# Kernel tuning notes

Hardware: AMD Instinct MI355X
Metric: run time of the kernel (lower is better)

The kernel has to match this reference:

```python
import jax, jax.numpy as jnp
import numpy as np

N = 200000; E = 800000; B = 4096; L = 512
DIN = 64; DE = 16; H = 128; PD = 1152


def setup_inputs() -> dict:
    key = jax.random.key(0)
    ks = jax.random.split(key, 40)
    def nrm(k, shape, fan_in):
        return jax.random.normal(k, shape, jnp.float32) * (1.0 / np.sqrt(fan_in))
    inp = {}
    inp['x'] = jax.random.normal(ks[0], (N, DIN), jnp.float32)
    inp['edge_index'] = jax.random.randint(ks[1], (2, E), 0, N, dtype=jnp.int32)
    inp['edge_attr'] = jax.random.normal(ks[2], (E, DE), jnp.float32)
    inp['batch'] = jnp.sort(jax.random.randint(ks[3], (N,), 0, B, dtype=jnp.int32))
    # 6 expert blocks: [0,1]=shared, [2,3]=sars, [4,5]=mers
    inp['eW1'] = nrm(ks[4], (6, DIN, H), DIN); inp['ea_s1'] = nrm(ks[5], (6, H), H)
    inp['ea_d1'] = nrm(ks[6], (6, H), H); inp['eWe1'] = nrm(ks[7], (6, DE, H), DE)
    inp['ea_e1'] = nrm(ks[8], (6, H), H); inp['eb1'] = jnp.zeros((6, H), jnp.float32)
    inp['bn1_g'] = jnp.ones((6, H), jnp.float32); inp['bn1_b'] = jnp.zeros((6, H), jnp.float32)
    inp['eW2'] = nrm(ks[9], (6, H, H), H); inp['ea_s2'] = nrm(ks[10], (6, H), H)
    inp['ea_d2'] = nrm(ks[11], (6, H), H); inp['eWe2'] = nrm(ks[12], (6, DE, H), DE)
    inp['ea_e2'] = nrm(ks[13], (6, H), H); inp['eb2'] = jnp.zeros((6, H), jnp.float32)
    inp['bn2_g'] = jnp.ones((6, H), jnp.float32); inp['bn2_b'] = jnp.zeros((6, H), jnp.float32)
    # gates (one GATConv with 4 output channels per task)
    inp['gW'] = nrm(ks[14], (2, DIN, 4), DIN); inp['ga_s'] = nrm(ks[15], (2, 4), 4)
    inp['ga_d'] = nrm(ks[16], (2, 4), 4); inp['gWe'] = nrm(ks[17], (2, DE, 4), DE)
    inp['ga_e'] = nrm(ks[18], (2, 4), 4); inp['gb'] = jnp.zeros((2, 4), jnp.float32)
    # cross-modal attention per task + frozen protein embeddings
    inp['Wq'] = nrm(ks[19], (2, H, H), H)
    inp['Wk'] = nrm(ks[20], (2, PD, H), PD)
    inp['Wv'] = nrm(ks[21], (2, PD, H), PD)
    inp['pe'] = jax.random.normal(ks[22], (2, L, PD), jnp.float32)
    # task heads
    inp['Wh1'] = nrm(ks[23], (2, 2 * H, H), 2 * H); inp['bh1'] = jnp.zeros((2, H), jnp.float32)
    inp['hbn_g'] = jnp.ones((2, H), jnp.float32); inp['hbn_b'] = jnp.zeros((2, H), jnp.float32)
    inp['Wh2'] = nrm(ks[24], (2, H, 1), H); inp['bh2'] = jnp.zeros((2, 1), jnp.float32)
    return inp


def _gat(x, src, dst, eattr, W, a_s, a_d, We, a_e, b):
    # PyG GATConv (heads=1, edge_dim set): shared linear for src/dst.
    h = x @ W                                   # [N, C]
    l = (h @ a_s)[src] + (h @ a_d)[dst] + (eattr @ We) @ a_e  # [E]
    l = jax.nn.leaky_relu(l, 0.2)
    m = jax.ops.segment_max(l, dst, num_segments=N)
    m = jnp.where(jnp.isfinite(m), m, 0.0)
    ex = jnp.exp(l - m[dst])
    den = jax.ops.segment_sum(ex, dst, num_segments=N)
    alpha = ex / (den[dst] + 1e-16)             # edge softmax over incoming edges
    return jax.ops.segment_sum(alpha[:, None] * h[src], dst, num_segments=N) + b


def _gat_multi(x, src, dst, eattr, W, a_s, a_d, We, a_e, b):
    # gate GATConv outputs C>1 channels with heads=1 -> same scalar-alpha math
    return _gat(x, src, dst, eattr, W, a_s, a_d, We, a_e, b)


def _bn(x, g, b):
    mu = jnp.mean(x, axis=0)
    var = jnp.var(x, axis=0)
    return (x - mu) * jax.lax.rsqrt(var + 1e-5) * g + b


def reference(x, edge_index, edge_attr, batch,
              eW1, ea_s1, ea_d1, eWe1, ea_e1, eb1, bn1_g, bn1_b,
              eW2, ea_s2, ea_d2, eWe2, ea_e2, eb2, bn2_g, bn2_b,
              gW, ga_s, ga_d, gWe, ga_e, gb,
              Wq, Wk, Wv, pe, Wh1, bh1, hbn_g, hbn_b, Wh2, bh2):
    src, dst = edge_index[0], edge_index[1]

    def expert(i):
        h = _gat(x, src, dst, edge_attr, eW1[i], ea_s1[i], ea_d1[i], eWe1[i], ea_e1[i], eb1[i])
        h = jax.nn.leaky_relu(_bn(h, bn1_g[i], bn1_b[i]), 0.01)
        h = _gat(h, src, dst, edge_attr, eW2[i], ea_s2[i], ea_d2[i], eWe2[i], ea_e2[i], eb2[i])
        return jax.nn.leaky_relu(_bn(h, bn2_g[i], bn2_b[i]), 0.01)

    reps = [expert(i) for i in range(6)]  # each [N, H]

    preds = []
    for t in range(2):
        # merged experts: shared then task-specific (cat order in torch code)
        merged = jnp.stack([reps[0], reps[1], reps[2 + 2 * t], reps[3 + 2 * t]], axis=1)  # [N,4,H]
        glog = _gat_multi(x, src, dst, edge_attr, gW[t], ga_s[t], ga_d[t], gWe[t], ga_e[t], gb[t])
        gate = jax.nn.softmax(glog, axis=1)                     # [N,4]
        node = jnp.einsum('neh,ne->nh', merged, gate)           # CGC combine
        pooled = jax.ops.segment_sum(node, batch, num_segments=B)  # global_add_pool [B,H]
        Q = pooled @ Wq[t]                                      # [B,H]
        K = pe[t] @ Wk[t]                                       # [L,H]
        V = pe[t] @ Wv[t]
        attn = jax.nn.softmax(Q @ K.T / jnp.sqrt(jnp.float32(H)), axis=-1)
        ctx = attn @ V
        fused = jnp.concatenate([pooled, ctx], axis=1)          # [B,2H]
        hh = jax.nn.leaky_relu(_bn(fused @ Wh1[t] + bh1[t], hbn_g[t], hbn_b[t]), 0.01)
        preds.append(hh @ Wh2[t] + bh2[t])
    return jnp.concatenate(preds, axis=1)  # [B,2]
```

## Files before the change

### kernel.cpp

```cpp
#include <hip/hip_runtime.h>
#include <hip/hip_bf16.h>
#include <cstdint>
#include <cstddef>
#include <type_traits>

constexpr int DIN = 64;
constexpr int DE  = 16;
constexpr int H   = 128;
constexpr int L   = 512;
constexpr int PD  = 1152;
constexpr int NBSTAT = 2048;

using bf16 = __hip_bfloat16;
typedef __attribute__((ext_vector_type(8))) short short8;
typedef __attribute__((ext_vector_type(4))) float float4v;

__device__ __forceinline__ float bflo(unsigned u) { return __uint_as_float(u << 16); }
__device__ __forceinline__ float bfhi(unsigned u) { return __uint_as_float(u & 0xffff0000u); }
__device__ __forceinline__ unsigned short f2b(float f) {
  bf16 h = __float2bfloat16(f);
  return *reinterpret_cast<unsigned short*>(&h);
}
__device__ __forceinline__ unsigned pack2(float a, float b) {
  return (unsigned)f2b(a) | ((unsigned)f2b(b) << 16);
}

__global__ void k_zero_i32(int* p, int n) {
  int i = blockIdx.x * 256 + threadIdx.x;
  if (i < n) p[i] = 0;
}
__global__ void k_zero_f32(float* p, int n) {
  int i = blockIdx.x * 256 + threadIdx.x;
  if (i < n) p[i] = 0.f;
}

__global__ void k_cvt_bf16(const float* __restrict__ in, bf16* __restrict__ out, int npairs) {
  int i = blockIdx.x * 256 + threadIdx.x;
  if (i >= npairs) return;
  float2 v = ((const float2*)in)[i];
  ((unsigned*)out)[i] = pack2(v.x, v.y);
}

__global__ void k_deg(const int* __restrict__ dst, int* __restrict__ deg, int e) {
  int i = blockIdx.x * 256 + threadIdx.x;
  if (i < e) atomicAdd(&deg[dst[i]], 1);
}

__global__ void k_scan1(const int* __restrict__ deg, int* __restrict__ out,
                        int* __restrict__ bsum, int n) {
  __shared__ int tmp[512];
  int tid = threadIdx.x;
  int i = blockIdx.x * 512 + tid;
  int v = (i < n) ? deg[i] : 0;
  tmp[tid] = v; __syncthreads();
  for (int s = 1; s < 512; s <<= 1) {
    int t = (tid >= s) ? tmp[tid - s] : 0;
    __syncthreads();
    tmp[tid] += t;
    __syncthreads();
  }
  if (i < n) out[i] = tmp[tid] - v;
  if (tid == 511) bsum[blockIdx.x] = tmp[511];
}

__global__ void k_scan2(int* bsum, int nb) {
  __shared__ int tmp[512];
  int tid = threadIdx.x;
  int v = (tid < nb) ? bsum[tid] : 0;
  tmp[tid] = v; __syncthreads();
  for (int s = 1; s < 512; s <<= 1) {
    int t = (tid >= s) ? tmp[tid - s] : 0;
    __syncthreads();
    tmp[tid] += t;
    __syncthreads();
  }
  if (tid < nb) bsum[tid] = tmp[tid] - v;
}

__global__ void k_scan3(int* __restrict__ off, const int* __restrict__ bsum,
                        int* __restrict__ cursor, int n, int total) {
  int i = blockIdx.x * 512 + threadIdx.x;
  if (i < n) { int v = off[i] + bsum[blockIdx.x]; off[i] = v; cursor[i] = v; }
  if (i == 0) off[n] = total;
}

__global__ void k_fill(const int* __restrict__ dst, int* __restrict__ cursor,
                       int* __restrict__ eid, int e) {
  int i = blockIdx.x * 256 + threadIdx.x;
  if (i < e) { int slot = atomicAdd(&cursor[dst[i]], 1); eid[slot] = i; }
}

__global__ void k_weall(const float* __restrict__ gWe, const float* __restrict__ ga_e,
                        const float* __restrict__ eWe1, const float* __restrict__ ea_e1,
                        const float* __restrict__ eWe2, const float* __restrict__ ea_e2,
                        float* __restrict__ weall) {
  int tid = threadIdx.x;
  if (tid >= 14 * 16) return;
  int c = tid >> 4, j = tid & 15;
  float acc = 0.f;
  if (c < 2) {
    for (int k = 0; k < 4; ++k) acc += gWe[(c * 16 + j) * 4 + k] * ga_e[c * 4 + k];
  } else if (c < 8) {
    int i = c - 2;
    for (int k = 0; k < 128; ++k) acc += eWe1[(i * 16 + j) * 128 + k] * ea_e1[i * 128 + k];
  } else {
    int i = c - 8;
    for (int k = 0; k < 128; ++k) acc += eWe2[(i * 16 + j) * 128 + k] * ea_e2[i * 128 + k];
  }
  weall[c * 16 + j] = acc;
}

__global__ void k_wpackall(const float* __restrict__ eW1, const float* __restrict__ eW2,
                           bf16* __restrict__ Wp1, bf16* __restrict__ Wp2) {
  int tid = blockIdx.x * 256 + threadIdx.x;
  const int L1TOT = 6 * 8192;
  if (tid < L1TOT) {
    int i = tid / 8192, r = tid % 8192;
    int kt = r / 4096, nt = (r / 512) & 7, l = (r / 8) & 63, j = r & 7;
    int k = kt * 32 + (l >> 4) * 8 + j, col = nt * 16 + (l & 15);
    Wp1[tid] = __float2bfloat16(eW1[(size_t)i * 64 * 128 + k * 128 + col]);
  } else {
    int t2 = tid - L1TOT;
    if (t2 >= 6 * 16384) return;
    int i = t2 / 16384, r = t2 % 16384;
    int kt = r / 4096, nt = (r / 512) & 7, l = (r / 8) & 63, j = r & 7;
    int k = kt * 32 + (l >> 4) * 8 + j, col = nt * 16 + (l & 15);
    Wp2[t2] = __float2bfloat16(eW2[(size_t)i * 128 * 128 + k * 128 + col]);
  }
}

__global__ void k_csrprep(const int* __restrict__ eid, const int* __restrict__ src,
                          const int* __restrict__ dst, const float* __restrict__ eattr,
                          const float* __restrict__ weall, int* __restrict__ src_csr,
                          int* __restrict__ dst_csr, float* __restrict__ edots, int e) {
  __shared__ float w[14 * 16];
  if (threadIdx.x < 14 * 16) w[threadIdx.x] = weall[threadIdx.x];
  __syncthreads();
  int i = blockIdx.x * 256 + threadIdx.x;
  if (i >= e) return;
  int ed = eid[i];
  src_csr[i] = src[ed];
  dst_csr[i] = dst[ed];
  float ea[16];
  const float4* ep = (const float4*)(eattr + (size_t)ed * 16);
#pragma unroll
  for (int q = 0; q < 4; ++q) {
    float4 v = ep[q];
    ea[q * 4] = v.x; ea[q * 4 + 1] = v.y; ea[q * 4 + 2] = v.z; ea[q * 4 + 3] = v.w;
  }
#pragma unroll
  for (int c = 0; c < 14; ++c) {
    float acc = 0.f;
#pragma unroll
    for (int j = 0; j < 16; ++j) acc += ea[j] * w[c * 16 + j];
    edots[(size_t)c * e + i] = acc;
  }
}

template <int K, bool BN>
__global__ __launch_bounds__(256) void k_mfma_gemm(
    const bf16* __restrict__ A, const bf16* __restrict__ Wp,
    const float* __restrict__ a_s, const float* __restrict__ a_d,
    bf16* __restrict__ out, float* __restrict__ s, float* __restrict__ d, int n,
    const float* __restrict__ bnsums, const float* __restrict__ bng,
    const float* __restrict__ bnb, float invn) {
  constexpr int KT = K / 32;
  __shared__ bf16 At[64][K + 8];
  __shared__ float sscale[128], sshift[128];
  if (BN) {
    if (threadIdx.x < K) {
      int c = threadIdx.x;
      float mu = bnsums[c] * invn;
      float var = bnsums[128 + c] * invn - mu * mu;
      float sc = rsqrtf(var + 1e-5f) * bng[c];
      sscale[c] = sc;
      sshift[c] = bnb[c] - mu * sc;
    }
    __syncthreads();
  }
  int row0 = blockIdx.x * 64;
  const int vecPerRow = K / 8;
  for (int idx = threadIdx.x; idx < 64 * vecPerRow; idx += 256) {
    int r = idx / vecPerRow, v = idx - r * vecPerRow;
    int gr = row0 + r;
    uint4 u = {0u, 0u, 0u, 0u};
    if (gr < n) u = ((const uint4*)(A + (size_t)gr * K))[v];
    if (BN) {
      float f[8] = {bflo(u.x), bfhi(u.x), bflo(u.y), bfhi(u.y),
                    bflo(u.z), bfhi(u.z), bflo(u.w), bfhi(u.w)};
      int c0 = v * 8;
#pragma unroll
      for (int j = 0; j < 8; ++j) {
        float y = f[j] * sscale[c0 + j] + sshift[c0 + j];
        f[j] = (y > 0.f) ? y : 0.01f * y;
      }
      u.x = pack2(f[0], f[1]); u.y = pack2(f[2], f[3]);
      u.z = pack2(f[4], f[5]); u.w = pack2(f[6], f[7]);
    }
    *((uint4*)&At[r][v * 8]) = u;
  }
  __syncthreads();
  int lane = threadIdx.x & 63, w = threadIdx.x >> 6;
  int c = lane & 15, q = lane >> 4;
  int wrow = w * 16;
  short8 afrag[KT];
#pragma unroll
  for (int kt = 0; kt < KT; ++kt)
    afrag[kt] = *(const short8*)&At[wrow + c][kt * 32 + q * 8];
  const short8* wp8 = (const short8*)Wp;
  float4v acc[8];
#pragma unroll
  for (int nt = 0; nt < 8; ++nt) acc[nt] = {0.f, 0.f, 0.f, 0.f};
#pragma unroll
  for (int kt = 0; kt < KT; ++kt) {
#pragma unroll
    for (int nt = 0; nt < 8; ++nt) {
      short8 bfrag = wp8[(kt * 8 + nt) * 64 + lane];
      acc[nt] = __builtin_amdgcn_mfma_f32_16x16x32_bf16(afrag[kt], bfrag, acc[nt], 0, 0, 0);
    }
  }
#pragma unroll
  for (int nt = 0; nt < 8; ++nt) {
#pragma unroll
    for (int reg = 0; reg < 4; ++reg) {
      int gr = row0 + wrow + q * 4 + reg;
      if (gr < n) out[(size_t)gr * 128 + nt * 16 + c] = __float2bfloat16(acc[nt][reg]);
    }
  }
#pragma unroll
  for (int reg = 0; reg < 4; ++reg) {
    float vs = 0.f, vd = 0.f;
#pragma unroll
    for (int nt = 0; nt < 8; ++nt) {
      float y = acc[nt][reg];
      int col = nt * 16 + c;
      vs += y * a_s[col];
      vd += y * a_d[col];
    }
#pragma unroll
    for (int o = 1; o < 16; o <<= 1) { vs += __shfl_xor(vs, o); vd += __shfl_xor(vd, o); }
    int gr = row0 + wrow + q * 4 + reg;
    if (c == 0 && gr < n) { s[gr] = vs; d[gr] = vd; }
  }
}

__global__ void k_edge_l(const int* __restrict__ src_csr, const int* __restrict__ dst_csr,
                         const float* __restrict__ edot, const float* __restrict__ s,
                         const float* __restrict__ d, float* __restrict__ lcsr, int e) {
  int i = blockIdx.x * 256 + threadIdx.x;
  if (i >= e) return;
  float l = s[src_csr[i]] + d[dst_csr[i]] + edot[i];
  lcsr[i] = (l > 0.f) ? l : 0.2f * l;
}

__global__ void k_agg128(const int* __restrict__ off, const int* __restrict__ src_csr,
                         const float* __restrict__ lcsr, const bf16* __restrict__ feat,
                         const float* __restrict__ bias, bf16* __restrict__ out, int n) {
  int node = blockIdx.x * 8 + (threadIdx.x >> 5);
  int lane = threadIdx.x & 31;
  if (node >= n) return;
  int e0 = off[node], e1 = off[node + 1];
  float m = -INFINITY;
  for (int i = e0 + lane; i < e1; i += 32) m = fmaxf(m, lcsr[i]);
  for (int o = 16; o; o >>= 1) m = fmaxf(m, __shfl_xor(m, o));
  float den = 0.f;
  for (int i = e0 + lane; i < e1; i += 32) den += __expf(lcsr[i] - m);
  for (int o = 16; o; o >>= 1) den += __shfl_xor(den, o);
  float inv = 1.0f / (den + 1e-16f);
  float4 acc = {0.f, 0.f, 0.f, 0.f};
  for (int i = e0; i < e1; ++i) {
    float alpha = __expf(lcsr[i] - m) * inv;
    const uint2* fr = (const uint2*)(feat + (size_t)src_csr[i] * 128);
    uint2 u = fr[lane];
    acc.x += alpha * bflo(u.x);
    acc.y += alpha * bfhi(u.x);
    acc.z += alpha * bflo(u.y);
    acc.w += alpha * bfhi(u.y);
  }
  float4 b4 = ((const float4*)bias)[lane];
  uint2 o2;
  o2.x = pack2(acc.x + b4.x, acc.y + b4.y);
  o2.y = pack2(acc.z + b4.z, acc.w + b4.w);
  ((uint2*)(out + (size_t)node * 128))[lane] = o2;
}

__global__ void k_gfeat(const float* __restrict__ x, const float* __restrict__ W,
                        const float* __restrict__ a_s, const float* __restrict__ a_d,
                        float* __restrict__ gfeat, float* __restrict__ s,
                        float* __restrict__ d, int n) {
  int i = blockIdx.x * 256 + threadIdx.x;
  if (i >= n) return;
  const float* xr = x + (size_t)i * DIN;
  float acc[4] = {0.f, 0.f, 0.f, 0.f};
  for (int k = 0; k < DIN; ++k) {
    float xv = xr[k];
#pragma unroll
    for (int j = 0; j < 4; ++j) acc[j] += xv * W[k * 4 + j];
  }
  float ss = 0.f, dd = 0.f;
#pragma unroll
  for (int j = 0; j < 4; ++j) {
    gfeat[(size_t)i * 4 + j] = acc[j];
    ss += acc[j] * a_s[j];
    dd += acc[j] * a_d[j];
  }
  s[i] = ss; d[i] = dd;
}

__global__ void k_agg4(const int* __restrict__ off, const int* __restrict__ src_csr,
                       const float* __restrict__ lcsr, const float* __restrict__ gfeat,
                       const float* __restrict__ bias, float* __restrict__ gates, int n) {
  int node = blockIdx.x * 256 + threadIdx.x;
  if (node >= n) return;
  int e0 = off[node], e1 = off[node + 1];
  float m = -INFINITY;
  for (int i = e0; i < e1; ++i) m = fmaxf(m, lcsr[i]);
  float den = 0.f;
  for (int i = e0; i < e1; ++i) den += __expf(lcsr[i] - m);
  float inv = 1.f / (den + 1e-16f);
  float4 acc = {0.f, 0.f, 0.f, 0.f};
  for (int i = e0; i < e1; ++i) {
    float a = __expf(lcsr[i] - m) * inv;
    float4 fr = *((const float4*)(gfeat + (size_t)src_csr[i] * 4));
    acc.x += a * fr.x; acc.y += a * fr.y; acc.z += a * fr.z; acc.w += a * fr.w;
  }
  float b0 = bias[0], b1 = bias[1], b2 = bias[2], b3 = bias[3];
  acc.x += b0; acc.y += b1; acc.z += b2; acc.w += b3;
  float mm = fmaxf(fmaxf(acc.x, acc.y), fmaxf(acc.z, acc.w));
  float e0s = __expf(acc.x - mm), e1s = __expf(acc.y - mm);
  float e2s = __expf(acc.z - mm), e3s = __expf(acc.w - mm);
  float is = 1.f / (e0s + e1s + e2s + e3s);
  float4 g4 = {e0s * is, e1s * is, e2s * is, e3s * is};
  *((float4*)(gates + (size_t)node * 4)) = g4;
}

__global__ __launch_bounds__(256) void k_bnstats_part(const bf16* __restrict__ x,
                                                      float* __restrict__ partials, int n) {
  __shared__ float sm[16 * 128];
  __shared__ float sq[16 * 128];
  int t = threadIdx.x;
  int g = t & 15;
  int slot = t >> 4;
  float s[8], q[8];
#pragma unroll
  for (int j = 0; j < 8; ++j) { s[j] = 0.f; q[j] = 0.f; }
  for (int r = blockIdx.x * 16 + slot; r < n; r += gridDim.x * 16) {
    uint4 u = ((const uint4*)(x + (size_t)r * 128))[g];
    float f[8] = {bflo(u.x), bfhi(u.x), bflo(u.y), bfhi(u.y),
                  bflo(u.z), bfhi(u.z), bflo(u.w), bfhi(u.w)};
#pragma unroll
    for (int j = 0; j < 8; ++j) { s[j] += f[j]; q[j] += f[j] * f[j]; }
  }
#pragma unroll
  for (int j = 0; j < 8; ++j) {
    sm[slot * 128 + g * 8 + j] = s[j];
    sq[slot * 128 + g * 8 + j] = q[j];
  }
  __syncthreads();
  if (t < 128) {
    float a = 0.f, b = 0.f;
#pragma unroll
    for (int sl = 0; sl < 16; ++sl) { a += sm[sl * 128 + t]; b += sq[sl * 128 + t]; }
    partials[(size_t)blockIdx.x * 256 + t] = a;
    partials[(size_t)blockIdx.x * 256 + 128 + t] = b;
  }
}

__global__ void k_bnstats_fin(const float* __restrict__ partials, float* __restrict__ sums,
                              int nblk) {
  int t = threadIdx.x;
  int cl = t >> 5, sl = t & 31;
  int ch = blockIdx.x * 8 + cl;
  float a = 0.f, b = 0.f;
  for (int blk = sl; blk < nblk; blk += 32) {
    a += partials[(size_t)blk * 256 + ch];
    b += partials[(size_t)blk * 256 + 128 + ch];
  }
#pragma unroll
  for (int o = 16; o; o >>= 1) { a += __shfl_xor(a, o); b += __shfl_xor(b, o); }
  if (sl == 0) { sums[ch] = a; sums[128 + ch] = b; }
}

__global__ void k_bnstats_f32(const float* __restrict__ x, float* __restrict__ sums,
                              float* __restrict__ sumsq, int n) {
  __shared__ float s1[256], s2[256];
  int c = threadIdx.x & 127, half = threadIdx.x >> 7;
  float a = 0.f, b = 0.f;
  for (int r = blockIdx.x * 2 + half; r < n; r += gridDim.x * 2) {
    float v = x[(size_t)r * 128 + c];
    a += v; b += v * v;
  }
  s1[threadIdx.x] = a; s2[threadIdx.x] = b;
  __syncthreads();
  if (half == 0) {
    atomicAdd(&sums[c], s1[c] + s1[c + 128]);
    atomicAdd(&sumsq[c], s2[c] + s2[c + 128]);
  }
}

__global__ void k_poolexpert(const bf16* __restrict__ x, const float* __restrict__ sums,
                             const float* __restrict__ sumsq, const float* __restrict__ g,
                             const float* __restrict__ bb, const int* __restrict__ batch,
                             const float* __restrict__ gates0, int slot0,
                             const float* __restrict__ gates1, int slot1,
                             float* __restrict__ pooled0, float* __restrict__ pooled1,
                             int n, float invn) {
  int b = blockIdx.x, t = threadIdx.x;
  int lo = 0, hi = n;
  while (lo < hi) { int m = (lo + hi) >> 1; if (batch[m] < b) lo = m + 1; else hi = m; }
  int start = lo;
  lo = start; hi = n;
  while (lo < hi) { int m = (lo + hi) >> 1; if (batch[m] < b + 1) lo = m + 1; else hi = m; }
  int end = lo;
  int c0 = 2 * t, c1 = 2 * t + 1;
  float mu0 = sums[c0] * invn, mu1 = sums[c1] * invn;
  float sc0 = rsqrtf(sumsq[c0] * invn - mu0 * mu0 + 1e-5f) * g[c0];
  float sc1 = rsqrtf(sumsq[c1] * invn - mu1 * mu1 + 1e-5f) * g[c1];
  float sh0 = bb[c0], sh1 = bb[c1];
  float a00 = 0.f, a01 = 0.f, a10 = 0.f, a11 = 0.f;
  for (int r = start; r < end; ++r) {
    unsigned u = ((const unsigned*)(x + (size_t)r * 128))[t];
    float y0 = (bflo(u) - mu0) * sc0 + sh0;
    float y1 = (bfhi(u) - mu1) * sc1 + sh1;
    y0 = (y0 > 0.f) ? y0 : 0.01f * y0;
    y1 = (y1 > 0.f) ? y1 : 0.01f * y1;
    if (slot0 >= 0) {
      float gw = gates0[(size_t)r * 4 + slot0];
      a00 += gw * y0; a01 += gw * y1;
    }
    if (slot1 >= 0) {
      float gw = gates1[(size_t)r * 4 + slot1];
      a10 += gw * y0; a11 += gw * y1;
    }
  }
  if (slot0 >= 0) {
    pooled0[(size_t)b * 128 + c0] += a00;
    pooled0[(size_t)b * 128 + c1] += a01;
  }
  if (slot1 >= 0) {
    pooled1[(size_t)b * 128 + c0] += a10;
    pooled1[(size_t)b * 128 + c1] += a11;
  }
}

__global__ void k_kv(const float* __restrict__ pe, const float* __restrict__ Wk,
                     const float* __restrict__ Wv, float* __restrict__ Kt,
                     float* __restrict__ Vout) {
  __shared__ float per[PD];
  int l = blockIdx.x, c = threadIdx.x;
  for (int p = threadIdx.x; p < PD; p += 128) per[p] = pe[(size_t)l * PD + p];
  __syncthreads();
  float ak = 0.f, av = 0.f;
  for (int p = 0; p < PD; ++p) {
    float v = per[p];
    ak += v * Wk[p * 128 + c];
    av += v * Wv[p * 128 + c];
  }
  Kt[(size_t)c * L + l] = ak;
  Vout[(size_t)l * 128 + c] = av;
}

__global__ void k_rowgemm(const float* __restrict__ in, const float* __restrict__ W,
                          float* __restrict__ out, int Kdim) {
  __shared__ float rr[256];
  int row = blockIdx.x, c = threadIdx.x;
  for (int k = threadIdx.x; k < Kdim; k += 128) rr[k] = in[(size_t)row * Kdim + k];
  __syncthreads();
  float acc = 0.f;
  for (int k = 0; k < Kdim; ++k) acc += rr[k] * W[k * 128 + c];
  out[(size_t)row * 128 + c] = acc;
}

__global__ void k_attn(const float* __restrict__ Q, const float* __restrict__ Kt,
                       const float* __restrict__ Vm, float* __restrict__ ctx) {
  __shared__ float q[4][128];
  __shared__ float sc[4][L];
  __shared__ float4 red[128];
  __shared__ float4 Mg, Ig;
  int b0 = blockIdx.x * 4, t = threadIdx.x;
#pragma unroll
  for (int g = 0; g < 4; ++g) q[g][t] = Q[(size_t)(b0 + g) * 128 + t];
  __syncthreads();
  float acc[4][4];
#pragma unroll
  for (int g = 0; g < 4; ++g)
#pragma unroll
    for (int j = 0; j < 4; ++j) acc[g][j] = 0.f;
  for (int k = 0; k < 128; ++k) {
    const float* kr = Kt + (size_t)k * L + t;
    float k0 = kr[0], k1 = kr[128], k2 = kr[256], k3 = kr[384];
#pragma unroll
    for (int g = 0; g < 4; ++g) {
      float qv = q[g][k];
      acc[g][0] += qv * k0; acc[g][1] += qv * k1;
      acc[g][2] += qv * k2; acc[g][3] += qv * k3;
    }
  }
  const float scale = 0.08838834764831845f;
  float4 pm;
  {
    float m[4];
#pragma unroll
    for (int g = 0; g < 4; ++g) {
#pragma unroll
      for (int j = 0; j < 4; ++j) {
        acc[g][j] *= scale;
        sc[g][t + j * 128] = acc[g][j];
      }
      m[g] = fmaxf(fmaxf(acc[g][0], acc[g][1]), fmaxf(acc[g][2], acc[g][3]));
    }
    pm = {m[0], m[1], m[2], m[3]};
  }
  red[t] = pm; __syncthreads();
  for (int s = 64; s > 0; s >>= 1) {
    if (t < s) {
      float4 o = red[t + s];
      red[t].x = fmaxf(red[t].x, o.x); red[t].y = fmaxf(red[t].y, o.y);
      red[t].z = fmaxf(red[t].z, o.z); red[t].w = fmaxf(red[t].w, o.w);
    }
    __syncthreads();
  }
  if (t == 0) Mg = red[0];
  __syncthreads();
  float4 M = Mg;
  float4 ps = {0, 0, 0, 0};
#pragma unroll
  for (int g = 0; g < 4; ++g) {
    float mg = (g == 0) ? M.x : (g == 1) ? M.y : (g == 2) ? M.z : M.w;
    float sgsum = 0.f;
#pragma unroll
    for (int j = 0; j < 4; ++j) {
      float e = __expf(acc[g][j] - mg);
      sc[g][t + j * 128] = e;
      sgsum += e;
    }
    if (g == 0) ps.x = sgsum; else if (g == 1) ps.y = sgsum;
    else if (g == 2) ps.z = sgsum; else ps.w = sgsum;
  }
  __syncthreads();
  red[t] = ps; __syncthreads();
  for (int s = 64; s > 0; s >>= 1) {
    if (t < s) {
      float4 o = red[t + s];
      red[t].x += o.x; red[t].y += o.y; red[t].z += o.z; red[t].w += o.w;
    }
    __syncthreads();
  }
  if (t == 0) Ig = {1.f / red[0].x, 1.f / red[0].y, 1.f / red[0].z, 1.f / red[0].w};
  __syncthreads();
  float4 I = Ig;
  float o0 = 0.f, o1 = 0.f, o2 = 0.f, o3 = 0.f;
  for (int l = 0; l < L; ++l) {
    float v = Vm[(size_t)l * 128 + t];
    o0 += sc[0][l] * v; o1 += sc[1][l] * v; o2 += sc[2][l] * v; o3 += sc[3][l] * v;
  }
  ctx[(size_t)(b0 + 0) * 128 + t] = o0 * I.x;
  ctx[(size_t)(b0 + 1) * 128 + t] = o1 * I.y;
  ctx[(size_t)(b0 + 2) * 128 + t] = o2 * I.z;
  ctx[(size_t)(b0 + 3) * 128 + t] = o3 * I.w;
}

__global__ void k_head1(const float* __restrict__ pooled, const float* __restrict__ ctx,
                        const float* __restrict__ Wh1, const float* __restrict__ bh1,
                        float* __restrict__ hh) {
  __shared__ float f[256];
  int b = blockIdx.x, c = threadIdx.x;
  f[c] = pooled[(size_t)b * 128 + c];
  f[c + 128] = ctx[(size_t)b * 128 + c];
  __syncthreads();
  float acc = bh1[c];
  for (int k = 0; k < 256; ++k) acc += f[k] * Wh1[k * 128 + c];
  hh[(size_t)b * 128 + c] = acc;
}

__global__ void k_head2(const float* __restrict__ hh, const float* __restrict__ sums,
                        const float* __restrict__ sumsq, const float* __restrict__ g,
                        const float* __restrict__ bbn, const float* __restrict__ Wh2,
                        const float* __restrict__ bh2, float* __restrict__ out, int t,
                        float invn) {
  __shared__ float red[2];
  int b = blockIdx.x, c = threadIdx.x;
  float mu = sums[c] * invn;
  float var = sumsq[c] * invn - mu * mu;
  float y = (hh[(size_t)b * 128 + c] - mu) * rsqrtf(var + 1e-5f) * g[c] + bbn[c];
  y = (y > 0.f) ? y : 0.01f * y;
  float p = y * Wh2[c];
  for (int o = 32; o; o >>= 1) p += __shfl_down(p, o);
  if ((threadIdx.x & 63) == 0) red[threadIdx.x >> 6] = p;
  __syncthreads();
  if (threadIdx.x == 0) out[(size_t)b * 2 + t] = red[0] + red[1] + bh2[0];
}

extern "C" void kernel_launch(void* const* d_in, const int* in_sizes, int n_in,
                              void* d_out, int out_size, void* d_ws, size_t ws_size,
                              hipStream_t stream) {
  (void)n_in; (void)ws_size;
  const float* x     = (const float*)d_in[0];
  const int*   eidx  = (const int*)d_in[1];
  const float* eattr = (const float*)d_in[2];
  const int*   batch = (const int*)d_in[3];
  const float* eW1   = (const float*)d_in[4];
  const float* ea_s1 = (const float*)d_in[5];
  const float* ea_d1 = (const float*)d_in[6];
  const float* eWe1  = (const float*)d_in[7];
  const float* ea_e1 = (const float*)d_in[8];
  const float* eb1   = (const float*)d_in[9];
  const float* bn1_g = (const float*)d_in[10];
  const float* bn1_b = (const float*)d_in[11];
  const float* eW2   = (const float*)d_in[12];
  const float* ea_s2 = (const float*)d_in[13];
  const float* ea_d2 = (const float*)d_in[14];
  const float* eWe2  = (const float*)d_in[15];
  const float* ea_e2 = (const float*)d_in[16];
  const float* eb2   = (const float*)d_in[17];
  const float* bn2_g = (const float*)d_in[18];
  const float* bn2_b = (const float*)d_in[19];
  const float* gW    = (const float*)d_in[20];
  const float* ga_s  = (const float*)d_in[21];
  const float* ga_d  = (const float*)d_in[22];
  const float* gWe   = (const float*)d_in[23];
  const float* ga_e  = (const float*)d_in[24];
  const float* gb    = (const float*)d_in[25];
  const float* Wq    = (const float*)d_in[26];
  const float* Wk    = (const float*)d_in[27];
  const float* Wv    = (const float*)d_in[28];
  const float* pe    = (const float*)d_in[29];
  const float* Wh1   = (const float*)d_in[30];
  const float* bh1   = (const float*)d_in[31];
  const float* hbn_g = (const float*)d_in[32];
  const float* hbn_b = (const float*)d_in[33];
  const float* Wh2   = (const float*)d_in[34];
  const float* bh2   = (const float*)d_in[35];
  float* out = (float*)d_out;

  const int n = in_sizes[0] / DIN;
  const int e = in_sizes[1] / 2;
  const int nb_graphs = out_size / 2;
  const int* src = eidx;
  const int* dst = eidx + e;

  char* p = (char*)d_ws;
  auto carve = [&](size_t bytes) {
    void* r = (void*)p;
    p += (bytes + 255) & ~(size_t)255;
    return r;
  };
  int* deg       = (int*)carve((size_t)n * 4);
  int* off       = (int*)carve(((size_t)n + 1) * 4);
  int* cursor    = (int*)carve((size_t)n * 4);
  int* eid       = (int*)carve((size_t)e * 4);
  int* bsum      = (int*)carve(4096);
  int* src_csr   = (int*)carve((size_t)e * 4);
  int* dst_csr   = (int*)carve((size_t)e * 4);
  float* edots   = (float*)carve((size_t)14 * e * 4);
  float* weall   = (float*)carve(14 * 16 * 4);
  float* s_arr   = (float*)carve((size_t)n * 4);
  float* d_arr   = (float*)carve((size_t)n * 4);
  float* lcsr    = (float*)carve((size_t)e * 4);
  float* sums    = (float*)carve(256 * 4);
  float* partials = (float*)carve((size_t)NBSTAT * 256 * 4);
  float* gates0  = (float*)carve((size_t)n * 16);
  float* gates1  = (float*)carve((size_t)n * 16);
  float* gfeat   = (float*)carve((size_t)n * 16);
  float* pooled0 = (float*)carve((size_t)nb_graphs * H * 4);
  float* pooled1 = (float*)carve((size_t)nb_graphs * H * 4);
  float* Ktbuf   = (float*)carve((size_t)L * H * 4);
  float* Vbuf    = (float*)carve((size_t)L * H * 4);
  float* Qbuf    = (float*)carve((size_t)nb_graphs * H * 4);
  float* ctxb    = (float*)carve((size_t)nb_graphs * H * 4);
  float* hhb     = (float*)carve((size_t)nb_graphs * H * 4);
  bf16* featbuf  = (bf16*)carve((size_t)n * H * 2);
  bf16* buf1     = (bf16*)carve((size_t)n * H * 2);
  bf16* xbf      = (bf16*)carve((size_t)n * DIN * 2);
  bf16* Wp1      = (bf16*)carve((size_t)6 * 8192 * 2);
  bf16* Wp2      = (bf16*)carve((size_t)6 * 16384 * 2);

  float invn = 1.0f / n;

  k_cvt_bf16<<<(n * DIN / 2 + 255) / 256, 256, 0, stream>>>(x, xbf, n * DIN / 2);
  k_wpackall<<<(6 * 8192 + 6 * 16384 + 255) / 256, 256, 0, stream>>>(eW1, eW2, Wp1, Wp2);

  k_zero_i32<<<(n + 255) / 256, 256, 0, stream>>>(deg, n);
  k_deg<<<(e + 255) / 256, 256, 0, stream>>>(dst, deg, e);
  int nsb = (n + 511) / 512;
  k_scan1<<<nsb, 512, 0, stream>>>(deg, off, bsum, n);
  k_scan2<<<1, 512, 0, stream>>>(bsum, nsb);
  k_scan3<<<nsb, 512, 0, stream>>>(off, bsum, cursor, n, e);
  k_fill<<<(e + 255) / 256, 256, 0, stream>>>(dst, cursor, eid, e);

  k_weall<<<1, 256, 0, stream>>>(gWe, ga_e, eWe1, ea_e1, eWe2, ea_e2, weall);
  k_csrprep<<<(e + 255) / 256, 256, 0, stream>>>(eid, src, dst, eattr, weall, src_csr,
                                                 dst_csr, edots, e);

  for (int t = 0; t < 2; ++t) {
    float* gates = t ? gates1 : gates0;
    k_gfeat<<<(n + 255) / 256, 256, 0, stream>>>(x, gW + t * DIN * 4, ga_s + t * 4,
                                                 ga_d + t * 4, gfeat, s_arr, d_arr, n);
    k_edge_l<<<(e + 255) / 256, 256, 0, stream>>>(src_csr, dst_csr, edots + (size_t)t * e,
                                                  s_arr, d_arr, lcsr, e);
    k_agg4<<<(n + 255) / 256, 256, 0, stream>>>(off, src_csr, lcsr, gfeat, gb + t * 4,
                                                gates, n);
  }

  k_zero_f32<<<(nb_graphs * H + 255) / 256, 256, 0, stream>>>(pooled0, nb_graphs * H);
  k_zero_f32<<<(nb_graphs * H + 255) / 256, 256, 0, stream>>>(pooled1, nb_graphs * H);

  int gblk = (n + 63) / 64;
  for (int i = 0; i < 6; ++i) {
    k_mfma_gemm<DIN, false><<<gblk, 256, 0, stream>>>(
        xbf, Wp1 + (size_t)i * 8192, ea_s1 + i * H, ea_d1 + i * H, featbuf, s_arr, d_arr,
        n, nullptr, nullptr, nullptr, 0.f);
    k_edge_l<<<(e + 255) / 256, 256, 0, stream>>>(src_csr, dst_csr,
                                                  edots + (size_t)(2 + i) * e, s_arr,
                                                  d_arr, lcsr, e);
    k_agg128<<<(n + 7) / 8, 256, 0, stream>>>(off, src_csr, lcsr, featbuf, eb1 + i * H,
                                              buf1, n);
    k_bnstats_part<<<NBSTAT, 256, 0, stream>>>(buf1, partials, n);
    k_bnstats_fin<<<16, 256, 0, stream>>>(partials, sums, NBSTAT);
    k_mfma_gemm<H, true><<<gblk, 256, 0, stream>>>(
        buf1, Wp2 + (size_t)i * 16384, ea_s2 + i * H, ea_d2 + i * H, featbuf, s_arr,
        d_arr, n, sums, bn1_g + i * H, bn1_b + i * H, invn);
    k_edge_l<<<(e + 255) / 256, 256, 0, stream>>>(src_csr, dst_csr,
                                                  edots + (size_t)(8 + i) * e, s_arr,
                                                  d_arr, lcsr, e);
    k_agg128<<<(n + 7) / 8, 256, 0, stream>>>(off, src_csr, lcsr, featbuf, eb2 + i * H,
                                              buf1, n);
    k_bnstats_part<<<NBSTAT, 256, 0, stream>>>(buf1, partials, n);
    k_bnstats_fin<<<16, 256, 0, stream>>>(partials, sums, NBSTAT);
    int s0 = (i < 4) ? i : -1;
    int s1 = (i < 2) ? i : (i >= 4 ? i - 2 : -1);
    k_poolexpert<<<nb_graphs, 64, 0, stream>>>(buf1, sums, sums + 128, bn2_g + i * H,
                                               bn2_b + i * H, batch, gates0, s0, gates1,
                                               s1, pooled0, pooled1, n, invn);
  }

  for (int t = 0; t < 2; ++t) {
    const float* pooled = t ? pooled1 : pooled0;
    k_kv<<<L, 128, 0, stream>>>(pe + (size_t)t * L * PD, Wk + t * PD * H, Wv + t * PD * H,
                                Ktbuf, Vbuf);
    k_rowgemm<<<nb_graphs, 128, 0, stream>>>(pooled, Wq + t * H * H, Qbuf, H);
    k_attn<<<nb_graphs / 4, 128, 0, stream>>>(Qbuf, Ktbuf, Vbuf, ctxb);
    k_head1<<<nb_graphs, 128, 0, stream>>>(pooled, ctxb, Wh1 + t * 2 * H * H, bh1 + t * H,
                                           hhb);
    k_zero_f32<<<1, 256, 0, stream>>>(sums, 256);
    k_bnstats_f32<<<64, 256, 0, stream>>>(hhb, sums, sums + 128, nb_graphs);
    k_head2<<<nb_graphs, 128, 0, stream>>>(hhb, sums, sums + 128, hbn_g + t * H,
                                           hbn_b + t * H, Wh2 + t * H, bh2 + t, out, t,
                                           1.0f / nb_graphs);
  }
}
```

Measured before the change: 2.795 ms.

## Fuse BatchNorm statistics into GAT aggregation with wave-per-node edge-parallel gather

The separate BN partial-statistics pass over the aggregated output is folded into the GAT aggregation kernel, so each block accumulates per-channel sum and sum-of-squares while writing results. This removes a full re-read of the N×128 bf16 buffer and one launch per layer. The aggregation is also restructured: a 64-lane wave handles one node, four lane groups each process different edges with 16-byte gathers, and the partial sums are combined with shuffles. The kernel now uses a fixed persistent grid with a grid-stride loop. The risk is lower parallelism for high-degree nodes, plus possible precision differences because stats now come from fp32 values rather than rounded bf16.

Result: slower. 3.199 ms (+14.5%).

```diff
diff --git a/kernel.cpp b/kernel.cpp
--- a/kernel.cpp
+++ b/kernel.cpp
@@ -9,7 +9,7 @@
 constexpr int H   = 128;
 constexpr int L   = 512;
 constexpr int PD  = 1152;
-constexpr int NBSTAT = 2048;
+constexpr int NAGG = 2048;
 
 using bf16 = __hip_bfloat16;
 typedef __attribute__((ext_vector_type(8))) short short8;
@@ -253,35 +253,70 @@
   lcsr[i] = (l > 0.f) ? l : 0.2f * l;
 }
 
-__global__ void k_agg128(const int* __restrict__ off, const int* __restrict__ src_csr,
-                         const float* __restrict__ lcsr, const bf16* __restrict__ feat,
-                         const float* __restrict__ bias, bf16* __restrict__ out, int n) {
-  int node = blockIdx.x * 8 + (threadIdx.x >> 5);
-  int lane = threadIdx.x & 31;
-  if (node >= n) return;
-  int e0 = off[node], e1 = off[node + 1];
-  float m = -INFINITY;
-  for (int i = e0 + lane; i < e1; i += 32) m = fmaxf(m, lcsr[i]);
-  for (int o = 16; o; o >>= 1) m = fmaxf(m, __shfl_xor(m, o));
-  float den = 0.f;
-  for (int i = e0 + lane; i < e1; i += 32) den += __expf(lcsr[i] - m);
-  for (int o = 16; o; o >>= 1) den += __shfl_xor(den, o);
-  float inv = 1.0f / (den + 1e-16f);
-  float4 acc = {0.f, 0.f, 0.f, 0.f};
-  for (int i = e0; i < e1; ++i) {
-    float alpha = __expf(lcsr[i] - m) * inv;
-    const uint2* fr = (const uint2*)(feat + (size_t)src_csr[i] * 128);
-    uint2 u = fr[lane];
-    acc.x += alpha * bflo(u.x);
-    acc.y += alpha * bfhi(u.x);
-    acc.z += alpha * bflo(u.y);
-    acc.w += alpha * bfhi(u.y);
-  }
-  float4 b4 = ((const float4*)bias)[lane];
-  uint2 o2;
-  o2.x = pack2(acc.x + b4.x, acc.y + b4.y);
-  o2.y = pack2(acc.z + b4.z, acc.w + b4.w);
-  ((uint2*)(out + (size_t)node * 128))[lane] = o2;
+__global__ __launch_bounds__(256) void k_agg128s(
+    const int* __restrict__ off, const int* __restrict__ src_csr,
+    const float* __restrict__ lcsr, const bf16* __restrict__ feat,
+    const float* __restrict__ bias, bf16* __restrict__ out,
+    float* __restrict__ partials, int n) {
+  __shared__ float sm[4][128], sq[4][128];
+  int w = threadIdx.x >> 6, lane = threadIdx.x & 63;
+  int g = lane >> 4, h = lane & 15;
+  float b8[8];
+#pragma unroll
+  for (int j = 0; j < 8; ++j) b8[j] = bias[h * 8 + j];
+  float sum8[8], sq8[8];
+#pragma unroll
+  for (int j = 0; j < 8; ++j) { sum8[j] = 0.f; sq8[j] = 0.f; }
+  int stride = gridDim.x * 4;
+  for (int node = blockIdx.x * 4 + w; node < n; node += stride) {
+    int e0 = off[node], e1 = off[node + 1];
+    float m = -INFINITY;
+    for (int i = e0 + lane; i < e1; i += 64) m = fmaxf(m, lcsr[i]);
+#pragma unroll
+    for (int o = 32; o; o >>= 1) m = fmaxf(m, __shfl_xor(m, o));
+    float den = 0.f;
+    for (int i = e0 + lane; i < e1; i += 64) den += __expf(lcsr[i] - m);
+#pragma unroll
+    for (int o = 32; o; o >>= 1) den += __shfl_xor(den, o);
+    float inv = 1.f / (den + 1e-16f);
+    float acc[8];
+#pragma unroll
+    for (int j = 0; j < 8; ++j) acc[j] = 0.f;
+    for (int i = e0 + g; i < e1; i += 4) {
+      float alpha = __expf(lcsr[i] - m) * inv;
+      uint4 u = ((const uint4*)(feat + (size_t)src_csr[i] * 128))[h];
+      acc[0] += alpha * bflo(u.x); acc[1] += alpha * bfhi(u.x);
+      acc[2] += alpha * bflo(u.y); acc[3] += alpha * bfhi(u.y);
+      acc[4] += alpha * bflo(u.z); acc[5] += alpha * bfhi(u.z);
+      acc[6] += alpha * bflo(u.w); acc[7] += alpha * bfhi(u.w);
+    }
+#pragma unroll
+    for (int j = 0; j < 8; ++j) {
+      acc[j] += __shfl_xor(acc[j], 16);
+      acc[j] += __shfl_xor(acc[j], 32);
+      acc[j] += b8[j];
+    }
+    if (g == 0) {
+      uint4 o4;
+      o4.x = pack2(acc[0], acc[1]); o4.y = pack2(acc[2], acc[3]);
+      o4.z = pack2(acc[4], acc[5]); o4.w = pack2(acc[6], acc[7]);
+      ((uint4*)(out + (size_t)node * 128))[h] = o4;
+#pragma unroll
+      for (int j = 0; j < 8; ++j) { sum8[j] += acc[j]; sq8[j] += acc[j] * acc[j]; }
+    }
+  }
+  if (g == 0) {
+#pragma unroll
+    for (int j = 0; j < 8; ++j) { sm[w][h * 8 + j] = sum8[j]; sq[w][h * 8 + j] = sq8[j]; }
+  }
+  __syncthreads();
+  if (threadIdx.x < 128) {
+    int c = threadIdx.x;
+    float a = sm[0][c] + sm[1][c] + sm[2][c] + sm[3][c];
+    float b = sq[0][c] + sq[1][c] + sq[2][c] + sq[3][c];
+    partials[(size_t)blockIdx.x * 256 + c] = a;
+    partials[(size_t)blockIdx.x * 256 + 128 + c] = b;
+  }
 }
 
 __global__ void k_gfeat(const float* __restrict__ x, const float* __restrict__ W,
@@ -332,38 +367,6 @@
   float is = 1.f / (e0s + e1s + e2s + e3s);
   float4 g4 = {e0s * is, e1s * is, e2s * is, e3s * is};
   *((float4*)(gates + (size_t)node * 4)) = g4;
-}
-
-__global__ __launch_bounds__(256) void k_bnstats_part(const bf16* __restrict__ x,
-                                                      float* __restrict__ partials, int n) {
-  __shared__ float sm[16 * 128];
-  __shared__ float sq[16 * 128];
-  int t = threadIdx.x;
-  int g = t & 15;
-  int slot = t >> 4;
-  float s[8], q[8];
-#pragma unroll
-  for (int j = 0; j < 8; ++j) { s[j] = 0.f; q[j] = 0.f; }
-  for (int r = blockIdx.x * 16 + slot; r < n; r += gridDim.x * 16) {
-    uint4 u = ((const uint4*)(x + (size_t)r * 128))[g];
-    float f[8] = {bflo(u.x), bfhi(u.x), bflo(u.y), bfhi(u.y),
-                  bflo(u.z), bfhi(u.z), bflo(u.w), bfhi(u.w)};
-#pragma unroll
-    for (int j = 0; j < 8; ++j) { s[j] += f[j]; q[j] += f[j] * f[j]; }
-  }
-#pragma unroll
-  for (int j = 0; j < 8; ++j) {
-    sm[slot * 128 + g * 8 + j] = s[j];
-    sq[slot * 128 + g * 8 + j] = q[j];
-  }
-  __syncthreads();
-  if (t < 128) {
-    float a = 0.f, b = 0.f;
-#pragma unroll
-    for (int sl = 0; sl < 16; ++sl) { a += sm[sl * 128 + t]; b += sq[sl * 128 + t]; }
-    partials[(size_t)blockIdx.x * 256 + t] = a;
-    partials[(size_t)blockIdx.x * 256 + 128 + t] = b;
-  }
 }
 
 __global__ void k_bnstats_fin(const float* __restrict__ partials, float* __restrict__ sums,
@@ -658,7 +661,7 @@
   float* d_arr   = (float*)carve((size_t)n * 4);
   float* lcsr    = (float*)carve((size_t)e * 4);
   float* sums    = (float*)carve(256 * 4);
-  float* partials = (float*)carve((size_t)NBSTAT * 256 * 4);
+  float* partials = (float*)carve((size_t)NAGG * 256 * 4);
   float* gates0  = (float*)carve((size_t)n * 16);
   float* gates1  = (float*)carve((size_t)n * 16);
   float* gfeat   = (float*)carve((size_t)n * 16);
@@ -713,20 +716,18 @@
     k_edge_l<<<(e + 255) / 256, 256, 0, stream>>>(src_csr, dst_csr,
                                                   edots + (size_t)(2 + i) * e, s_arr,
                                                   d_arr, lcsr, e);
-    k_agg128<<<(n + 7) / 8, 256, 0, stream>>>(off, src_csr, lcsr, featbuf, eb1 + i * H,
-                                              buf1, n);
-    k_bnstats_part<<<NBSTAT, 256, 0, stream>>>(buf1, partials, n);
-    k_bnstats_fin<<<16, 256, 0, stream>>>(partials, sums, NBSTAT);
+    k_agg128s<<<NAGG, 256, 0, stream>>>(off, src_csr, lcsr, featbuf, eb1 + i * H, buf1,
+                                        partials, n);
+    k_bnstats_fin<<<16, 256, 0, stream>>>(partials, sums, NAGG);
     k_mfma_gemm<H, true><<<gblk, 256, 0, stream>>>(
         buf1, Wp2 + (size_t)i * 16384, ea_s2 + i * H, ea_d2 + i * H, featbuf, s_arr,
         d_arr, n, sums, bn1_g + i * H, bn1_b + i * H, invn);
     k_edge_l<<<(e + 255) / 256, 256, 0, stream>>>(src_csr, dst_csr,
                                                   edots + (size_t)(8 + i) * e, s_arr,
                                                   d_arr, lcsr, e);
-    k_agg128<<<(n + 7) / 8, 256, 0, stream>>>(off, src_csr, lcsr, featbuf, eb2 + i * H,
-                                              buf1, n);
-    k_bnstats_part<<<NBSTAT, 256, 0, stream>>>(buf1, partials, n);
-    k_bnstats_fin<<<16, 256, 0, stream>>>(partials, sums, NBSTAT);
+    k_agg128s<<<NAGG, 256, 0, stream>>>(off, src_csr, lcsr, featbuf, eb2 + i * H, buf1,
+                                        partials, n);
+    k_bnstats_fin<<<16, 256, 0, stream>>>(partials, sums, NAGG);
     int s0 = (i < 4) ? i : -1;
     int s1 = (i < 2) ? i : (i >= 4 ? i - 2 : -1);
     k_poolexpert<<<nb_graphs, 64, 0, stream>>>(buf1, sums, sums + 128, bn2_g + i * H,
```
